# Performance work log

Measured on AMD Instinct MI355X. Metric: run time of the kernel, lower is better.

The kernel has to match this reference:

```python
import jax, jax.numpy as jnp
import numpy as np

NUM_USERS = 100000
USER_EMB_DIM = 64
PROC_DIM = 128          # Dense(128) embedding_processor
NUM_SHARDS = 16
MEM_SIZE = 512          # memory slots per shard
WORD_SIZE = 64
NUM_READS = 4
INPUT_SIZE = 256
B, S = 256, 128
IN_DIM = INPUT_SIZE + PROC_DIM  # combined controller input width


def setup_inputs() -> dict:
    key = jax.random.key(0)
    k = jax.random.split(key, 7)
    x = jax.random.normal(k[0], (B, S, INPUT_SIZE), dtype=jnp.float32)
    user_id = jax.random.randint(k[1], (B,), 0, NUM_USERS, dtype=jnp.int64)
    user_emb_table = jax.random.normal(k[2], (NUM_USERS, USER_EMB_DIM), dtype=jnp.float32) * 0.02
    W_proc = jax.random.normal(k[3], (USER_EMB_DIM, PROC_DIM), dtype=jnp.float32) * (1.0 / np.sqrt(USER_EMB_DIM))
    b_proc = jnp.zeros((PROC_DIM,), dtype=jnp.float32)
    # per-shard parameters: query projection + memory matrix (the shard's state)
    Wq = jax.random.normal(k[4], (NUM_SHARDS, IN_DIM, NUM_READS * WORD_SIZE), dtype=jnp.float32) * (1.0 / np.sqrt(IN_DIM))
    memory = jax.random.normal(k[5], (NUM_SHARDS, MEM_SIZE, WORD_SIZE), dtype=jnp.float32)
    return {"x": x, "user_id": user_id, "user_emb_table": user_emb_table,
            "W_proc": W_proc, "b_proc": b_proc, "Wq": Wq, "memory": memory}


def reference(x, user_id, user_emb_table, W_proc, b_proc, Wq, memory):
    # user embedding lookup + Dense processor
    ue = user_emb_table[user_id]                       # [B, E]
    pe = ue @ W_proc + b_proc                          # [B, PROC_DIM]
    # broadcast the processed embedding across the sequence and concat on features
    pe_seq = jnp.broadcast_to(pe[:, None, :], (x.shape[0], x.shape[1], pe.shape[-1]))
    combined = jnp.concatenate([x, pe_seq], axis=-1)   # [B, S, IN_DIM]
    # shard routing (irregular gather of per-shard params)
    sid = user_id % NUM_SHARDS                         # [B]
    Wq_g = Wq[sid]                                     # [B, IN_DIM, R*W]
    mem_g = memory[sid]                                # [B, M, W]
    # per-sample shard forward: content-based read
    q = jnp.einsum('bsi,bio->bso', combined, Wq_g)     # [B, S, R*W]
    q = q.reshape(q.shape[0], q.shape[1], NUM_READS, WORD_SIZE)
    scores = jnp.einsum('bsrw,bmw->bsrm', q, mem_g)    # [B, S, R, M]
    wts = jax.nn.softmax(scores, axis=-1)
    read_words = jnp.einsum('bsrm,bmw->bsrw', wts, mem_g)  # [B, S, R, W]
    # original code keeps final_states[-1] (last sample's state)
    final_state = wts[-1]                              # [S, R, M]
    return read_words, final_state
```

## Files before the change

### kernel.cpp

```cpp
#include <hip/hip_runtime.h>
#include <math.h>

#define BB 256
#define SSEQ 128
#define INPUT 256
#define PD 128
#define EE 64
#define RW 256
#define MM 512
#define WW 64
#define KD 384

typedef _Float16 half8 __attribute__((ext_vector_type(8)));
typedef __fp16 fp16x2 __attribute__((ext_vector_type(2)));
typedef float float4v __attribute__((ext_vector_type(4)));

#define LOG2E 1.44269504088896f
#define OUT1 8388608u

#define MEMT_OFF 65536
#define F32_OFF  131072
#define LDS_BYTES (131072 + 6144)
#define UE_O 0
#define PE_O 64
#define QPE_O 192
#define QP_O 448

union H8 { half8 h8; unsigned int u[4]; uint4 u4; };

__device__ __forceinline__ unsigned int pk2(float a, float b) {
    union { fp16x2 h; unsigned int u; } p;
    p.h = __builtin_amdgcn_cvt_pkrtz(a, b);
    return p.u;
}

__global__ void __launch_bounds__(1024, 4)
attn_kernel(const float* __restrict__ x, const int* __restrict__ user_id,
            const float* __restrict__ uet, const float* __restrict__ W_proc,
            const float* __restrict__ b_proc, const float* __restrict__ Wq,
            const float* __restrict__ memG, float* __restrict__ out)
{
    extern __shared__ char smraw[];
    unsigned short* smemu = (unsigned short*)smraw;
    unsigned int*   smw   = (unsigned int*)smraw;
    uint4*          sm128 = (uint4*)smraw;
    float*          smf   = (float*)(smraw + F32_OFF);

    const int t = threadIdx.x;
    const int b = blockIdx.x;
    const int lane = t & 63, wv = t >> 6;
    const int n16 = lane & 15, quad = lane >> 4;
    const int r = wv & 3, sq = wv >> 2;
    const int s0 = sq * 32;
    const int swz = n16 & 7;

    const int uid = user_id[b];
    const int sid = uid & 15;
    const float* memB = memG + (size_t)sid * (MM*WW);
    const float* wqX  = Wq + (size_t)sid * KD * RW;

    if (t < EE) smf[UE_O + t] = uet[(size_t)uid*EE + t];

    for (int i = 0; i < 32; ++i) {
        int idx = i*1024 + t;
        int n = idx & 255, kp = idx >> 8;
        float w0 = wqX[(size_t)(2*kp)    *RW + n];
        float w1 = wqX[(size_t)(2*kp + 1)*RW + n];
        smw[((((kp>>2)*256 + n) << 2) | (kp & 3))] = pk2(w0, w1);
    }
    __syncthreads();

    if (t < PD) {
        float a = b_proc[t];
        #pragma unroll
        for (int e = 0; e < EE; ++e) a = fmaf(smf[UE_O + e], W_proc[e*PD + t], a);
        smf[PE_O + t] = a;
    }
    __syncthreads();
    {
        int n = t & 255, h = t >> 8;
        float s = 0.f;
        const float* wr = wqX + (size_t)(256 + h*32)*RW + n;
        #pragma unroll 8
        for (int k = 0; k < 32; ++k) s = fmaf(smf[PE_O + h*32 + k], wr[(size_t)k*RW], s);
        smf[QP_O + h*256 + n] = s;
    }
    __syncthreads();
    if (t < 256) smf[QPE_O + t] = LOG2E * (smf[QP_O + t] + smf[QP_O + 256 + t]
                                         + smf[QP_O + 512 + t] + smf[QP_O + 768 + t]);
    __syncthreads();

    float4v qacc[4][2];
    #pragma unroll
    for (int mt = 0; mt < 4; ++mt)
        #pragma unroll
        for (int nt = 0; nt < 2; ++nt) qacc[mt][nt] = (float4v)0.f;

    const float* xB = x + (size_t)(b*SSEQ + s0) * INPUT;
    for (int kc = 0; kc < 8; ++kc) {
        H8 afr[4];
        #pragma unroll
        for (int mt = 0; mt < 4; ++mt)
            afr[mt].u4 = sm128[(kc*4 + quad)*256 + r*64 + mt*16 + n16];
        H8 bfr[2];
        #pragma unroll
        for (int nt = 0; nt < 2; ++nt) {
            const float* xg = xB + (size_t)(nt*16 + n16)*INPUT + kc*32 + quad*8;
            float4 a0 = *(const float4*)xg;
            float4 a1 = *(const float4*)(xg + 4);
            bfr[nt].u[0] = pk2(a0.x*LOG2E, a0.y*LOG2E);
            bfr[nt].u[1] = pk2(a0.z*LOG2E, a0.w*LOG2E);
            bfr[nt].u[2] = pk2(a1.x*LOG2E, a1.y*LOG2E);
            bfr[nt].u[3] = pk2(a1.z*LOG2E, a1.w*LOG2E);
        }
        #pragma unroll
        for (int mt = 0; mt < 4; ++mt)
            #pragma unroll
            for (int nt = 0; nt < 2; ++nt)
                qacc[mt][nt] = __builtin_amdgcn_mfma_f32_16x16x32_f16(afr[mt].h8, bfr[nt].h8, qacc[mt][nt], 0, 0, 0);
    }
    #pragma unroll
    for (int mt = 0; mt < 4; ++mt)
        #pragma unroll
        for (int reg = 0; reg < 4; ++reg) {
            float qv = smf[QPE_O + r*64 + mt*16 + quad*4 + reg];
            #pragma unroll
            for (int nt = 0; nt < 2; ++nt) qacc[mt][nt][reg] += qv;
        }
    unsigned int pkq[4][2][2];
    #pragma unroll
    for (int mt = 0; mt < 4; ++mt)
        #pragma unroll
        for (int nt = 0; nt < 2; ++nt) {
            pkq[mt][nt][0] = pk2(qacc[mt][nt][0], qacc[mt][nt][1]);
            pkq[mt][nt][1] = pk2(qacc[mt][nt][2], qacc[mt][nt][3]);
        }
    unsigned int bq[2][2][4];
    #pragma unroll
    for (int kc2 = 0; kc2 < 2; ++kc2)
        #pragma unroll
        for (int nt = 0; nt < 2; ++nt)
            #pragma unroll
            for (int p = 0; p < 4; ++p) {
                int qp = ((quad & 1) << 1) | (p >> 1);
                int src = n16 + (qp << 4);
                int sr = p & 1;
                int lo  = __shfl((int)pkq[kc2*2    ][nt][sr], src, 64);
                int hiv = __shfl((int)pkq[kc2*2 + 1][nt][sr], src, 64);
                bq[kc2][nt][p] = (unsigned int)((quad < 2) ? lo : hiv);
            }
    __syncthreads();

    for (int i = 0; i < 4; ++i) {
        int id = t + i*1024;
        int m = id >> 3, cw = id & 7;
        const float* g = memB + m*64 + cw*8;
        float4 a0 = *(const float4*)g;
        float4 a1 = *(const float4*)(g + 4);
        sm128[m*8 + (cw ^ (m & 7))] =
            make_uint4(pk2(a0.x,a0.y), pk2(a0.z,a0.w), pk2(a1.x,a1.y), pk2(a1.z,a1.w));
    }
    __syncthreads();
    for (int i = 0; i < 4; ++i) {
        int id = t + i*1024;
        int w = id & 63, cm = id >> 6;
        unsigned int uu[4];
        #pragma unroll
        for (int p = 0; p < 4; ++p) {
            int m0 = cm*8 + 2*p, m1 = m0 + 1;
            unsigned short lo = smemu[m0*64 + (((w>>3) ^ (m0&7))<<3) + (w&7)];
            unsigned short hi = smemu[m1*64 + (((w>>3) ^ (m1&7))<<3) + (w&7)];
            uu[p] = (unsigned int)lo | ((unsigned int)hi << 16);
        }
        sm128[(MEMT_OFF >> 4) + w*64 + (cm ^ (w & 7))] = make_uint4(uu[0],uu[1],uu[2],uu[3]);
    }
    __syncthreads();

    float4v Oa[4][2];
    #pragma unroll
    for (int wt = 0; wt < 4; ++wt)
        #pragma unroll
        for (int nt = 0; nt < 2; ++nt) Oa[wt][nt] = (float4v)0.f;
    float Ml[2] = {-1e30f, -1e30f}, llp[2] = {0.f, 0.f};

    for (int mtile = 0; mtile < 16; ++mtile) {
        float4v Sa[2][2];
        #pragma unroll
        for (int msub = 0; msub < 2; ++msub)
            #pragma unroll
            for (int nt = 0; nt < 2; ++nt) Sa[msub][nt] = (float4v)0.f;
        #pragma unroll
        for (int msub = 0; msub < 2; ++msub) {
            int m = mtile*32 + msub*16 + n16;
            #pragma unroll
            for (int kc2 = 0; kc2 < 2; ++kc2) {
                H8 af; af.u4 = sm128[m*8 + ((kc2*4 + quad) ^ swz)];
                #pragma unroll
                for (int nt = 0; nt < 2; ++nt) {
                    H8 bf; bf.u[0]=bq[kc2][nt][0]; bf.u[1]=bq[kc2][nt][1];
                           bf.u[2]=bq[kc2][nt][2]; bf.u[3]=bq[kc2][nt][3];
                    Sa[msub][nt] = __builtin_amdgcn_mfma_f32_16x16x32_f16(af.h8, bf.h8, Sa[msub][nt], 0, 0, 0);
                }
            }
        }
        unsigned int pkP[2][2][2];
        #pragma unroll
        for (int nt = 0; nt < 2; ++nt) {
            float tm = Sa[0][nt][0];
            #pragma unroll
            for (int g = 1; g < 4; ++g) tm = fmaxf(tm, Sa[0][nt][g]);
            #pragma unroll
            for (int g = 0; g < 4; ++g) tm = fmaxf(tm, Sa[1][nt][g]);
            tm = fmaxf(tm, __shfl_xor(tm, 16, 64));
            tm = fmaxf(tm, __shfl_xor(tm, 32, 64));
            float Mn = fmaxf(Ml[nt], tm);
            float al = __builtin_amdgcn_exp2f(Ml[nt] - Mn);
            float pv[2][4]; float ts = 0.f;
            #pragma unroll
            for (int msub = 0; msub < 2; ++msub)
                #pragma unroll
                for (int g = 0; g < 4; ++g) {
                    pv[msub][g] = __builtin_amdgcn_exp2f(Sa[msub][nt][g] - Mn);
                    ts += pv[msub][g];
                }
            llp[nt] = al*llp[nt] + ts;
            Ml[nt] = Mn;
            pkP[0][nt][0] = pk2(pv[0][0], pv[0][1]); pkP[0][nt][1] = pk2(pv[0][2], pv[0][3]);
            pkP[1][nt][0] = pk2(pv[1][0], pv[1][1]); pkP[1][nt][1] = pk2(pv[1][2], pv[1][3]);
            #pragma unroll
            for (int wt = 0; wt < 4; ++wt)
                #pragma unroll
                for (int g = 0; g < 4; ++g) Oa[wt][nt][g] *= al;
        }
        unsigned int bp[2][4];
        #pragma unroll
        for (int nt = 0; nt < 2; ++nt)
            #pragma unroll
            for (int p = 0; p < 4; ++p) {
                int qp = ((quad & 1) << 1) | (p >> 1);
                int src = n16 + (qp << 4);
                int sr = p & 1;
                int lo  = __shfl((int)pkP[0][nt][sr], src, 64);
                int hiv = __shfl((int)pkP[1][nt][sr], src, 64);
                bp[nt][p] = (unsigned int)((quad < 2) ? lo : hiv);
            }
        #pragma unroll
        for (int wt = 0; wt < 4; ++wt) {
            H8 af; af.u4 = sm128[(MEMT_OFF >> 4) + (wt*16 + n16)*64 + ((mtile*4 + quad) ^ swz)];
            #pragma unroll
            for (int nt = 0; nt < 2; ++nt) {
                H8 bf; bf.u[0]=bp[nt][0]; bf.u[1]=bp[nt][1]; bf.u[2]=bp[nt][2]; bf.u[3]=bp[nt][3];
                Oa[wt][nt] = __builtin_amdgcn_mfma_f32_16x16x32_f16(af.h8, bf.h8, Oa[wt][nt], 0, 0, 0);
            }
        }
    }

    float inv[2];
    #pragma unroll
    for (int nt = 0; nt < 2; ++nt) {
        float ll = llp[nt];
        ll += __shfl_xor(ll, 16, 64);
        ll += __shfl_xor(ll, 32, 64);
        inv[nt] = 1.0f / ll;
    }

    #pragma unroll
    for (int nt = 0; nt < 2; ++nt) {
        int s = s0 + nt*16 + n16;
        #pragma unroll
        for (int wt = 0; wt < 4; ++wt) {
            float4 o = make_float4(Oa[wt][nt][0]*inv[nt], Oa[wt][nt][1]*inv[nt],
                                   Oa[wt][nt][2]*inv[nt], Oa[wt][nt][3]*inv[nt]);
            *(float4*)&out[((size_t)(b*SSEQ + s)*4 + r)*WW + wt*16 + quad*4] = o;
        }
    }

    if (b == BB - 1) {
        for (int mtile = 0; mtile < 16; ++mtile) {
            float4v Sa[2][2];
            #pragma unroll
            for (int msub = 0; msub < 2; ++msub)
                #pragma unroll
                for (int nt = 0; nt < 2; ++nt) Sa[msub][nt] = (float4v)0.f;
            #pragma unroll
            for (int msub = 0; msub < 2; ++msub) {
                int m = mtile*32 + msub*16 + n16;
                #pragma unroll
                for (int kc2 = 0; kc2 < 2; ++kc2) {
                    H8 af; af.u4 = sm128[m*8 + ((kc2*4 + quad) ^ swz)];
                    #pragma unroll
                    for (int nt = 0; nt < 2; ++nt) {
                        H8 bf; bf.u[0]=bq[kc2][nt][0]; bf.u[1]=bq[kc2][nt][1];
                               bf.u[2]=bq[kc2][nt][2]; bf.u[3]=bq[kc2][nt][3];
                        Sa[msub][nt] = __builtin_amdgcn_mfma_f32_16x16x32_f16(af.h8, bf.h8, Sa[msub][nt], 0, 0, 0);
                    }
                }
            }
            #pragma unroll
            for (int nt = 0; nt < 2; ++nt) {
                int s = s0 + nt*16 + n16;
                size_t base = (size_t)OUT1 + ((size_t)(s*4 + r) << 9);
                #pragma unroll
                for (int msub = 0; msub < 2; ++msub) {
                    float4 w4 = make_float4(
                        __builtin_amdgcn_exp2f(Sa[msub][nt][0] - Ml[nt]) * inv[nt],
                        __builtin_amdgcn_exp2f(Sa[msub][nt][1] - Ml[nt]) * inv[nt],
                        __builtin_amdgcn_exp2f(Sa[msub][nt][2] - Ml[nt]) * inv[nt],
                        __builtin_amdgcn_exp2f(Sa[msub][nt][3] - Ml[nt]) * inv[nt]);
                    *(float4*)&out[base + mtile*32 + msub*16 + quad*4] = w4;
                }
            }
        }
    }
}

extern "C" void kernel_launch(void* const* d_in, const int* in_sizes, int n_in,
                              void* d_out, int out_size, void* d_ws, size_t ws_size,
                              hipStream_t stream) {
    const float* x    = (const float*)d_in[0];
    const int*   uid  = (const int*)  d_in[1];
    const float* uet  = (const float*)d_in[2];
    const float* Wp   = (const float*)d_in[3];
    const float* bp   = (const float*)d_in[4];
    const float* Wq   = (const float*)d_in[5];
    const float* mem  = (const float*)d_in[6];
    float* out = (float*)d_out;

    (void)hipFuncSetAttribute((const void*)attn_kernel,
                              hipFuncAttributeMaxDynamicSharedMemorySize, LDS_BYTES);
    attn_kernel<<<BB, 1024, LDS_BYTES, stream>>>(x, uid, uet, Wp, bp, Wq, mem, out);
}
```

Baseline: 167.1 us.

## Switch attention inner loop to 32x32x16 MFMA with permlane32 swaps

Replaces the 16x16x32 MFMA tiling of the score and read products with 32x32x16 MFMAs, so each wave handles 32 sequence rows by 32 memory slots per step. It also swaps the shuffle-based max/sum reductions and P operand repacking for permlane32_swap. The aim is fewer LDS operand loads, fewer shuffles and fewer softmax scalar ops per tile. In exchange it needs larger accumulator vectors (two 16-float outputs) and a changed data layout that must match the MFMA lane mapping.

Measured after the change: 164.8 us. No clear change (-1.4%).

```diff
diff --git a/kernel.cpp b/kernel.cpp
--- a/kernel.cpp
+++ b/kernel.cpp
@@ -14,11 +14,14 @@
 typedef _Float16 half8 __attribute__((ext_vector_type(8)));
 typedef __fp16 fp16x2 __attribute__((ext_vector_type(2)));
 typedef float float4v __attribute__((ext_vector_type(4)));
+typedef float f32x16 __attribute__((ext_vector_type(16)));
+typedef unsigned int uint2v __attribute__((ext_vector_type(2)));
 
 #define LOG2E 1.44269504088896f
 #define OUT1 8388608u
 
 #define MEMT_OFF 65536
+#define MEMT16   4096
 #define F32_OFF  131072
 #define LDS_BYTES (131072 + 6144)
 #define UE_O 0
@@ -32,6 +35,15 @@
     union { fp16x2 h; unsigned int u; } p;
     p.h = __builtin_amdgcn_cvt_pkrtz(a, b);
     return p.u;
+}
+
+__device__ __forceinline__ float xhalf_max(float v) {
+    uint2v r = __builtin_amdgcn_permlane32_swap(__float_as_uint(v), __float_as_uint(v), false, false);
+    return fmaxf(__uint_as_float(r[0]), __uint_as_float(r[1]));
+}
+__device__ __forceinline__ float xhalf_sum(float v) {
+    uint2v r = __builtin_amdgcn_permlane32_swap(__float_as_uint(v), __float_as_uint(v), false, false);
+    return __uint_as_float(r[0]) + __uint_as_float(r[1]);
 }
 
 __global__ void __launch_bounds__(1024, 4)
@@ -50,9 +62,10 @@
     const int b = blockIdx.x;
     const int lane = t & 63, wv = t >> 6;
     const int n16 = lane & 15, quad = lane >> 4;
+    const int l31 = lane & 31, hh = lane >> 5;
     const int r = wv & 3, sq = wv >> 2;
     const int s0 = sq * 32;
-    const int swz = n16 & 7;
+    const int mswz = l31 & 7;
 
     const int uid = user_id[b];
     const int sid = uid & 15;
@@ -135,20 +148,20 @@
             pkq[mt][nt][0] = pk2(qacc[mt][nt][0], qacc[mt][nt][1]);
             pkq[mt][nt][1] = pk2(qacc[mt][nt][2], qacc[mt][nt][3]);
         }
-    unsigned int bq[2][2][4];
-    #pragma unroll
-    for (int kc2 = 0; kc2 < 2; ++kc2)
-        #pragma unroll
-        for (int nt = 0; nt < 2; ++nt)
-            #pragma unroll
-            for (int p = 0; p < 4; ++p) {
-                int qp = ((quad & 1) << 1) | (p >> 1);
-                int src = n16 + (qp << 4);
-                int sr = p & 1;
-                int lo  = __shfl((int)pkq[kc2*2    ][nt][sr], src, 64);
-                int hiv = __shfl((int)pkq[kc2*2 + 1][nt][sr], src, 64);
-                bq[kc2][nt][p] = (unsigned int)((quad < 2) ? lo : hiv);
+    H8 bqf[4];
+    {
+        const int ntSel = (lane >> 4) & 1;
+        const int srcBase = (lane & 15) + (lane & 32);
+        #pragma unroll
+        for (int kc = 0; kc < 4; ++kc)
+            #pragma unroll
+            for (int jp = 0; jp < 4; ++jp) {
+                const int src = srcBase + ((jp >> 1) << 4);
+                int v0 = __shfl((int)pkq[kc][0][jp & 1], src, 64);
+                int v1 = __shfl((int)pkq[kc][1][jp & 1], src, 64);
+                bqf[kc].u[jp] = (unsigned int)(ntSel ? v1 : v0);
             }
+    }
     __syncthreads();
 
     for (int i = 0; i < 4; ++i) {
@@ -172,143 +185,91 @@
             unsigned short hi = smemu[m1*64 + (((w>>3) ^ (m1&7))<<3) + (w&7)];
             uu[p] = (unsigned int)lo | ((unsigned int)hi << 16);
         }
-        sm128[(MEMT_OFF >> 4) + w*64 + (cm ^ (w & 7))] = make_uint4(uu[0],uu[1],uu[2],uu[3]);
-    }
-    __syncthreads();
-
-    float4v Oa[4][2];
-    #pragma unroll
-    for (int wt = 0; wt < 4; ++wt)
-        #pragma unroll
-        for (int nt = 0; nt < 2; ++nt) Oa[wt][nt] = (float4v)0.f;
-    float Ml[2] = {-1e30f, -1e30f}, llp[2] = {0.f, 0.f};
+        sm128[MEMT16 + w*64 + (cm ^ (w & 7))] = make_uint4(uu[0],uu[1],uu[2],uu[3]);
+    }
+    __syncthreads();
+
+    f32x16 Oa0 = (f32x16)0.f, Oa1 = (f32x16)0.f;
+    float Ml = -1e30f, llp = 0.f;
 
     for (int mtile = 0; mtile < 16; ++mtile) {
-        float4v Sa[2][2];
-        #pragma unroll
-        for (int msub = 0; msub < 2; ++msub)
-            #pragma unroll
-            for (int nt = 0; nt < 2; ++nt) Sa[msub][nt] = (float4v)0.f;
-        #pragma unroll
-        for (int msub = 0; msub < 2; ++msub) {
-            int m = mtile*32 + msub*16 + n16;
-            #pragma unroll
-            for (int kc2 = 0; kc2 < 2; ++kc2) {
-                H8 af; af.u4 = sm128[m*8 + ((kc2*4 + quad) ^ swz)];
-                #pragma unroll
-                for (int nt = 0; nt < 2; ++nt) {
-                    H8 bf; bf.u[0]=bq[kc2][nt][0]; bf.u[1]=bq[kc2][nt][1];
-                           bf.u[2]=bq[kc2][nt][2]; bf.u[3]=bq[kc2][nt][3];
-                    Sa[msub][nt] = __builtin_amdgcn_mfma_f32_16x16x32_f16(af.h8, bf.h8, Sa[msub][nt], 0, 0, 0);
-                }
+        f32x16 Sa = (f32x16)0.f;
+        const int mrow = mtile*32 + l31;
+        #pragma unroll
+        for (int kc = 0; kc < 4; ++kc) {
+            H8 af; af.u4 = sm128[mrow*8 + (((kc<<1) + hh) ^ mswz)];
+            Sa = __builtin_amdgcn_mfma_f32_32x32x16_f16(af.h8, bqf[kc].h8, Sa, 0, 0, 0);
+        }
+        float tma = fmaxf(fmaxf(fmaxf(Sa[0],Sa[1]), fmaxf(Sa[2],Sa[3])),
+                          fmaxf(fmaxf(Sa[4],Sa[5]), fmaxf(Sa[6],Sa[7])));
+        float tmb = fmaxf(fmaxf(fmaxf(Sa[8],Sa[9]), fmaxf(Sa[10],Sa[11])),
+                          fmaxf(fmaxf(Sa[12],Sa[13]), fmaxf(Sa[14],Sa[15])));
+        float tm = xhalf_max(fmaxf(tma, tmb));
+        float Mn = fmaxf(Ml, tm);
+        float al = __builtin_amdgcn_exp2f(Ml - Mn);
+        float pv[16];
+        #pragma unroll
+        for (int g = 0; g < 16; ++g) pv[g] = __builtin_amdgcn_exp2f(Sa[g] - Mn);
+        float ts = (((pv[0]+pv[1])+(pv[2]+pv[3])) + ((pv[4]+pv[5])+(pv[6]+pv[7])))
+                 + (((pv[8]+pv[9])+(pv[10]+pv[11])) + ((pv[12]+pv[13])+(pv[14]+pv[15])));
+        llp = al*llp + ts;
+        Ml = Mn;
+        #pragma unroll
+        for (int g = 0; g < 16; ++g) { Oa0[g] *= al; Oa1[g] *= al; }
+        uint2v rA0 = __builtin_amdgcn_permlane32_swap(pk2(pv[0],pv[1]),   pk2(pv[4],pv[5]),   false, false);
+        uint2v rB0 = __builtin_amdgcn_permlane32_swap(pk2(pv[2],pv[3]),   pk2(pv[6],pv[7]),   false, false);
+        uint2v rA1 = __builtin_amdgcn_permlane32_swap(pk2(pv[8],pv[9]),   pk2(pv[12],pv[13]), false, false);
+        uint2v rB1 = __builtin_amdgcn_permlane32_swap(pk2(pv[10],pv[11]), pk2(pv[14],pv[15]), false, false);
+        H8 bp0; bp0.u[0]=rA0[0]; bp0.u[1]=rB0[0]; bp0.u[2]=rA0[1]; bp0.u[3]=rB0[1];
+        H8 bp1; bp1.u[0]=rA1[0]; bp1.u[1]=rB1[0]; bp1.u[2]=rA1[1]; bp1.u[3]=rB1[1];
+        const int c0 = mtile*4 + hh;
+        {
+            H8 af0; af0.u4 = sm128[MEMT16 + l31*64        + ( c0      ^ mswz)];
+            Oa0 = __builtin_amdgcn_mfma_f32_32x32x16_f16(af0.h8, bp0.h8, Oa0, 0, 0, 0);
+            H8 af1; af1.u4 = sm128[MEMT16 + l31*64        + ((c0 + 2) ^ mswz)];
+            Oa0 = __builtin_amdgcn_mfma_f32_32x32x16_f16(af1.h8, bp1.h8, Oa0, 0, 0, 0);
+            H8 af2; af2.u4 = sm128[MEMT16 + (32 + l31)*64 + ( c0      ^ mswz)];
+            Oa1 = __builtin_amdgcn_mfma_f32_32x32x16_f16(af2.h8, bp0.h8, Oa1, 0, 0, 0);
+            H8 af3; af3.u4 = sm128[MEMT16 + (32 + l31)*64 + ((c0 + 2) ^ mswz)];
+            Oa1 = __builtin_amdgcn_mfma_f32_32x32x16_f16(af3.h8, bp1.h8, Oa1, 0, 0, 0);
+        }
+    }
+
+    float inv = 1.0f / xhalf_sum(llp);
+
+    {
+        const int s = s0 + l31;
+        float* op = out + ((size_t)(b*SSEQ + s)*4 + r)*WW;
+        #pragma unroll
+        for (int rq = 0; rq < 4; ++rq) {
+            float4 o0 = make_float4(Oa0[rq*4+0]*inv, Oa0[rq*4+1]*inv,
+                                    Oa0[rq*4+2]*inv, Oa0[rq*4+3]*inv);
+            *(float4*)&op[rq*8 + hh*4] = o0;
+            float4 o1 = make_float4(Oa1[rq*4+0]*inv, Oa1[rq*4+1]*inv,
+                                    Oa1[rq*4+2]*inv, Oa1[rq*4+3]*inv);
+            *(float4*)&op[32 + rq*8 + hh*4] = o1;
+        }
+    }
+
+    if (b == BB - 1) {
+        const int s = s0 + l31;
+        size_t base = (size_t)OUT1 + ((size_t)(s*4 + r) << 9);
+        for (int mtile = 0; mtile < 16; ++mtile) {
+            f32x16 Sa = (f32x16)0.f;
+            const int mrow = mtile*32 + l31;
+            #pragma unroll
+            for (int kc = 0; kc < 4; ++kc) {
+                H8 af; af.u4 = sm128[mrow*8 + (((kc<<1) + hh) ^ mswz)];
+                Sa = __builtin_amdgcn_mfma_f32_32x32x16_f16(af.h8, bqf[kc].h8, Sa, 0, 0, 0);
             }
-        }
-        unsigned int pkP[2][2][2];
-        #pragma unroll
-        for (int nt = 0; nt < 2; ++nt) {
-            float tm = Sa[0][nt][0];
-            #pragma unroll
-            for (int g = 1; g < 4; ++g) tm = fmaxf(tm, Sa[0][nt][g]);
-            #pragma unroll
-            for (int g = 0; g < 4; ++g) tm = fmaxf(tm, Sa[1][nt][g]);
-            tm = fmaxf(tm, __shfl_xor(tm, 16, 64));
-            tm = fmaxf(tm, __shfl_xor(tm, 32, 64));
-            float Mn = fmaxf(Ml[nt], tm);
-            float al = __builtin_amdgcn_exp2f(Ml[nt] - Mn);
-            float pv[2][4]; float ts = 0.f;
-            #pragma unroll
-            for (int msub = 0; msub < 2; ++msub)
-                #pragma unroll
-                for (int g = 0; g < 4; ++g) {
-                    pv[msub][g] = __builtin_amdgcn_exp2f(Sa[msub][nt][g] - Mn);
-                    ts += pv[msub][g];
-                }
-            llp[nt] = al*llp[nt] + ts;
-            Ml[nt] = Mn;
-            pkP[0][nt][0] = pk2(pv[0][0], pv[0][1]); pkP[0][nt][1] = pk2(pv[0][2], pv[0][3]);
-            pkP[1][nt][0] = pk2(pv[1][0], pv[1][1]); pkP[1][nt][1] = pk2(pv[1][2], pv[1][3]);
-            #pragma unroll
-            for (int wt = 0; wt < 4; ++wt)
-                #pragma unroll
-                for (int g = 0; g < 4; ++g) Oa[wt][nt][g] *= al;
-        }
-        unsigned int bp[2][4];
-        #pragma unroll
-        for (int nt = 0; nt < 2; ++nt)
-            #pragma unroll
-            for (int p = 0; p < 4; ++p) {
-                int qp = ((quad & 1) << 1) | (p >> 1);
-                int src = n16 + (qp << 4);
-                int sr = p & 1;
-                int lo  = __shfl((int)pkP[0][nt][sr], src, 64);
-                int hiv = __shfl((int)pkP[1][nt][sr], src, 64);
-                bp[nt][p] = (unsigned int)((quad < 2) ? lo : hiv);
-            }
-        #pragma unroll
-        for (int wt = 0; wt < 4; ++wt) {
-            H8 af; af.u4 = sm128[(MEMT_OFF >> 4) + (wt*16 + n16)*64 + ((mtile*4 + quad) ^ swz)];
-            #pragma unroll
-            for (int nt = 0; nt < 2; ++nt) {
-                H8 bf; bf.u[0]=bp[nt][0]; bf.u[1]=bp[nt][1]; bf.u[2]=bp[nt][2]; bf.u[3]=bp[nt][3];
-                Oa[wt][nt] = __builtin_amdgcn_mfma_f32_16x16x32_f16(af.h8, bf.h8, Oa[wt][nt], 0, 0, 0);
-            }
-        }
-    }
-
-    float inv[2];
-    #pragma unroll
-    for (int nt = 0; nt < 2; ++nt) {
-        float ll = llp[nt];
-        ll += __shfl_xor(ll, 16, 64);
-        ll += __shfl_xor(ll, 32, 64);
-        inv[nt] = 1.0f / ll;
-    }
-
-    #pragma unroll
-    for (int nt = 0; nt < 2; ++nt) {
-        int s = s0 + nt*16 + n16;
-        #pragma unroll
-        for (int wt = 0; wt < 4; ++wt) {
-            float4 o = make_float4(Oa[wt][nt][0]*inv[nt], Oa[wt][nt][1]*inv[nt],
-                                   Oa[wt][nt][2]*inv[nt], Oa[wt][nt][3]*inv[nt]);
-            *(float4*)&out[((size_t)(b*SSEQ + s)*4 + r)*WW + wt*16 + quad*4] = o;
-        }
-    }
-
-    if (b == BB - 1) {
-        for (int mtile = 0; mtile < 16; ++mtile) {
-            float4v Sa[2][2];
-            #pragma unroll
-            for (int msub = 0; msub < 2; ++msub)
-                #pragma unroll
-                for (int nt = 0; nt < 2; ++nt) Sa[msub][nt] = (float4v)0.f;
-            #pragma unroll
-            for (int msub = 0; msub < 2; ++msub) {
-                int m = mtile*32 + msub*16 + n16;
-                #pragma unroll
-                for (int kc2 = 0; kc2 < 2; ++kc2) {
-                    H8 af; af.u4 = sm128[m*8 + ((kc2*4 + quad) ^ swz)];
-                    #pragma unroll
-                    for (int nt = 0; nt < 2; ++nt) {
-                        H8 bf; bf.u[0]=bq[kc2][nt][0]; bf.u[1]=bq[kc2][nt][1];
-                               bf.u[2]=bq[kc2][nt][2]; bf.u[3]=bq[kc2][nt][3];
-                        Sa[msub][nt] = __builtin_amdgcn_mfma_f32_16x16x32_f16(af.h8, bf.h8, Sa[msub][nt], 0, 0, 0);
-                    }
-                }
-            }
-            #pragma unroll
-            for (int nt = 0; nt < 2; ++nt) {
-                int s = s0 + nt*16 + n16;
-                size_t base = (size_t)OUT1 + ((size_t)(s*4 + r) << 9);
-                #pragma unroll
-                for (int msub = 0; msub < 2; ++msub) {
-                    float4 w4 = make_float4(
-                        __builtin_amdgcn_exp2f(Sa[msub][nt][0] - Ml[nt]) * inv[nt],
-                        __builtin_amdgcn_exp2f(Sa[msub][nt][1] - Ml[nt]) * inv[nt],
-                        __builtin_amdgcn_exp2f(Sa[msub][nt][2] - Ml[nt]) * inv[nt],
-                        __builtin_amdgcn_exp2f(Sa[msub][nt][3] - Ml[nt]) * inv[nt]);
-                    *(float4*)&out[base + mtile*32 + msub*16 + quad*4] = w4;
-                }
+            #pragma unroll
+            for (int rq = 0; rq < 4; ++rq) {
+                float4 w4 = make_float4(
+                    __builtin_amdgcn_exp2f(Sa[rq*4+0] - Ml) * inv,
+                    __builtin_amdgcn_exp2f(Sa[rq*4+1] - Ml) * inv,
+                    __builtin_amdgcn_exp2f(Sa[rq*4+2] - Ml) * inv,
+                    __builtin_amdgcn_exp2f(Sa[rq*4+3] - Ml) * inv);
+                *(float4*)&out[base + mtile*32 + rq*8 + hh*4] = w4;
             }
         }
     }
```
